# Kernel tuning notes

Hardware: AMD Instinct MI355X
Metric: run time of the kernel (lower is better)

## Reference

```python
import jax, jax.numpy as jnp
import numpy as np
import math

PI = math.pi
POS_RANGE = (0.0, PI, -PI, PI)            # (x_lo, x_hi, y_lo, y_hi)
DIR_RANGE = (0.5 * PI, 0.85 * PI, -0.85 * PI, -0.5 * PI)


def setup_inputs() -> dict:
    key = jax.random.key(0)
    kx, kg, kw1, kw2 = jax.random.split(key, 4)
    N = 1_048_576
    G0, G1, G2, G3, F = 64, 64, 32, 32, 16
    # sample query points strictly inside the valid angular ranges
    lo = jnp.array([POS_RANGE[0], POS_RANGE[2], DIR_RANGE[0], DIR_RANGE[2]], jnp.float32)
    hi = jnp.array([POS_RANGE[1], POS_RANGE[3], DIR_RANGE[1], DIR_RANGE[3]], jnp.float32)
    u = jax.random.uniform(kx, (N, 4), jnp.float32, 0.0, 0.999)
    x = lo + u * (hi - lo)
    # xavier-uniform learned 4D feature grid
    gb = math.sqrt(6.0 / (G3 + F))
    grid = jax.random.uniform(kg, (G0, G1, G2, G3, F), jnp.float32, -gb, gb)
    H = 4 * F
    b1v = math.sqrt(6.0 / (F + H))
    w1 = jax.random.uniform(kw1, (F, H), jnp.float32, -b1v, b1v)
    b1 = jnp.zeros((H,), jnp.float32)
    b2v = math.sqrt(6.0 / (H + 3))
    w2 = jax.random.uniform(kw2, (H, 3), jnp.float32, -b2v, b2v)
    b2 = jnp.zeros((3,), jnp.float32)
    return {"x": x, "grid": grid, "w1": w1, "b1": b1, "w2": w2, "b2": b2}


def _quadlinear(x, grid):
    G0, G1, G2, G3, F = grid.shape
    # normalize each coordinate to grid index space (faithful to original,
    # including normalizing dim0 by G0-1 / dim1 by G1-1 while dim0 indexes axis 1)
    c0 = (x[:, 0] - POS_RANGE[0]) / (POS_RANGE[1] - POS_RANGE[0]) * (G0 - 1)
    c1 = (x[:, 1] - POS_RANGE[2]) / (POS_RANGE[3] - POS_RANGE[2]) * (G1 - 1)
    c2 = (x[:, 2] - DIR_RANGE[0]) / (DIR_RANGE[1] - DIR_RANGE[0]) * (G2 - 1)
    c3 = (x[:, 3] - DIR_RANGE[2]) / (DIR_RANGE[3] - DIR_RANGE[2]) * (G3 - 1)
    W, H, D, T = G1 - 1, G0 - 1, G2 - 1, G3 - 1
    tlx = c0.astype(jnp.int32)  # coords are non-negative -> trunc == floor
    tly = c1.astype(jnp.int32)
    tlz = c2.astype(jnp.int32)
    tlw = c3.astype(jnp.int32)
    xf = jnp.mod(c0, 1.0)[:, None]
    yf = jnp.mod(c1, 1.0)[:, None]
    zf = jnp.mod(c2, 1.0)[:, None]
    wf = jnp.mod(c3, 1.0)[:, None]
    brx = jnp.minimum(tlx + 1, W)
    bry = jnp.minimum(tly + 1, H)
    brz = jnp.minimum(tlz + 1, D)
    brw = jnp.minimum(tlw + 1, T)
    g = lambda a, b, c, d: grid[a, b, c, d]  # [N, F] gather
    c0000 = g(tly, tlx, tlz, tlw); c1000 = g(tly, brx, tlz, tlw)
    c0100 = g(bry, tlx, tlz, tlw); c0010 = g(tly, tlx, brz, tlw)
    c0001 = g(tly, tlx, tlz, brw); c1100 = g(bry, brx, tlz, tlw)
    c1010 = g(tly, brx, brz, tlw); c1001 = g(tly, brx, tlz, brw)
    c0110 = g(bry, tlx, brz, tlw); c0101 = g(bry, tlx, tlz, brw)
    c0011 = g(tly, tlx, brz, brw); c1110 = g(bry, brx, brz, tlw)
    c1101 = g(bry, brx, tlz, brw); c1011 = g(tly, brx, brz, brw)
    c0111 = g(bry, tlx, brz, brw); c1111 = g(bry, brx, brz, brw)
    c00 = c0000 * (1 - xf) + c1000 * xf
    c01 = c0001 * (1 - xf) + c1001 * xf
    c10 = c0100 * (1 - xf) + c1100 * xf
    c11 = c0110 * (1 - xf) + c1110 * xf
    c20 = c0010 * (1 - xf) + c1010 * xf
    c21 = c0011 * (1 - xf) + c1011 * xf
    c30 = c0101 * (1 - xf) + c1101 * xf
    c31 = c0111 * (1 - xf) + c1111 * xf
    cc0 = c00 * (1 - yf) + c10 * yf
    cc1 = c01 * (1 - yf) + c11 * yf
    cc2 = c20 * (1 - yf) + c30 * yf
    cc3 = c21 * (1 - yf) + c31 * yf
    c4 = cc0 * (1 - zf) + cc2 * zf
    c5 = cc1 * (1 - zf) + cc3 * zf
    return c4 * (1 - wf) + c5 * wf  # [N, F]


def reference(x, grid, w1, b1, w2, b2):
    feat = _quadlinear(x, grid)
    h = feat @ w1 + b1
    h = jnp.where(h >= 0, h, 0.01 * h)  # LeakyReLU(0.01)
    out = h @ w2 + b2
    return jax.nn.sigmoid(out) * 255.0
```

## Files before the change

### kernel.cpp

```cpp
#include <hip/hip_runtime.h>
#include <math.h>

__global__ __launch_bounds__(256) void gridnet_kernel(
    const float* __restrict__ x,
    const float* __restrict__ grid,
    const float* __restrict__ w1,
    const float* __restrict__ b1,
    const float* __restrict__ w2,
    const float* __restrict__ b2,
    float* __restrict__ out,
    int N)
{
    __shared__ float w1s[16 * 64];
    __shared__ float b1s[64];
    __shared__ float w2s[64 * 3];
    __shared__ float b2s[4];

    const int t = threadIdx.x;
    for (int i = t; i < 1024; i += 256) w1s[i] = w1[i];
    if (t < 64)  b1s[t] = b1[t];
    if (t < 192) w2s[t] = w2[t];
    if (t < 3)   b2s[t] = b2[t];
    __syncthreads();

    const int gid = blockIdx.x * 256 + t;
    if (gid >= N) return;

    const float4 xv = reinterpret_cast<const float4*>(x)[gid];

    const float lo1 = (float)(-M_PI);
    const float sp0 = (float)(M_PI);
    const float sp1 = (float)(2.0 * M_PI);
    const float lo2 = (float)(0.5 * M_PI);
    const float sp2 = (float)(0.85 * M_PI - 0.5 * M_PI);
    const float lo3 = (float)(-0.85 * M_PI);
    const float sp3 = (float)(-0.5 * M_PI - (-0.85 * M_PI));

    const float c0 = (xv.x - 0.0f) / sp0 * 63.0f;
    const float c1 = (xv.y - lo1) / sp1 * 63.0f;
    const float c2 = (xv.z - lo2) / sp2 * 31.0f;
    const float c3 = (xv.w - lo3) / sp3 * 31.0f;

    const int tlx = (int)c0;
    const int tly = (int)c1;
    const int tlz = (int)c2;
    const int tlw = (int)c3;

    const float xf = c0 - (float)tlx;
    const float yf = c1 - (float)tly;
    const float zf = c2 - (float)tlz;
    const float wf = c3 - (float)tlw;

    const int brx = min(tlx + 1, 63);
    const int bry = min(tly + 1, 63);
    const int brz = min(tlz + 1, 31);
    const int brw = min(tlw + 1, 31);

    const float wx0 = 1.0f - xf, wx1 = xf;
    const float wy0 = 1.0f - yf, wy1 = yf;
    const float wz0 = 1.0f - zf, wz1 = zf;
    const float ww0 = 1.0f - wf, ww1 = wf;

    float cw[2][2][2];
    cw[0][0][0] = wy0 * wz0 * ww0;
    cw[0][0][1] = wy0 * wz0 * ww1;
    cw[0][1][0] = wy0 * wz1 * ww0;
    cw[0][1][1] = wy0 * wz1 * ww1;
    cw[1][0][0] = wy1 * wz0 * ww0;
    cw[1][0][1] = wy1 * wz1 * ww0;
    cw[1][1][0] = wy1 * wz0 * ww1;
    cw[1][1][1] = wy1 * wz1 * ww1;

    const float wxv[2] = {wx0, wx1};
    const int axv[2] = {tlx, brx};
    const int ayv[2] = {tly, bry};
    const int azv[2] = {tlz, brz};
    const int awv[2] = {tlw, brw};

    float feat[16];
    #pragma unroll
    for (int f = 0; f < 16; ++f) feat[f] = 0.0f;

    #pragma unroll
    for (int iy = 0; iy < 2; ++iy) {
        #pragma unroll
        for (int ix = 0; ix < 2; ++ix) {
            const int base1 = (ayv[iy] * 64 + axv[ix]) * 32;
            const float wyx = wxv[ix];
            #pragma unroll
            for (int iz = 0; iz < 2; ++iz) {
                const int base0 = (base1 + azv[iz]) * 32;
                #pragma unroll
                for (int iw = 0; iw < 2; ++iw) {
                    const float w = wyx * cw[iy][iz][iw];
                    const float4* p = reinterpret_cast<const float4*>(
                        grid + (size_t)(base0 + awv[iw]) * 16);
                    const float4 v0 = p[0];
                    const float4 v1 = p[1];
                    const float4 v2 = p[2];
                    const float4 v3 = p[3];
                    feat[0]  += w * v0.x;  feat[1]  += w * v0.y;
                    feat[2]  += w * v0.z;  feat[3]  += w * v0.w;
                    feat[4]  += w * v1.x;  feat[5]  += w * v1.y;
                    feat[6]  += w * v1.z;  feat[7]  += w * v1.w;
                    feat[8]  += w * v2.x;  feat[9]  += w * v2.y;
                    feat[10] += w * v2.z;  feat[11] += w * v2.w;
                    feat[12] += w * v3.x;  feat[13] += w * v3.y;
                    feat[14] += w * v3.z;  feat[15] += w * v3.w;
                }
            }
        }
    }

    float o0 = b2s[0];
    float o1 = b2s[1];
    float o2 = b2s[2];

    #pragma unroll
    for (int j4 = 0; j4 < 16; ++j4) {
        float4 h = reinterpret_cast<const float4*>(b1s)[j4];
        #pragma unroll
        for (int i = 0; i < 16; ++i) {
            const float4 wv = reinterpret_cast<const float4*>(w1s)[i * 16 + j4];
            h.x += feat[i] * wv.x;
            h.y += feat[i] * wv.y;
            h.z += feat[i] * wv.z;
            h.w += feat[i] * wv.w;
        }
        const float hx = (h.x >= 0.0f) ? h.x : 0.01f * h.x;
        const float hy = (h.y >= 0.0f) ? h.y : 0.01f * h.y;
        const float hz = (h.z >= 0.0f) ? h.z : 0.01f * h.z;
        const float hw = (h.w >= 0.0f) ? h.w : 0.01f * h.w;
        const float* w2p = w2s + j4 * 12;
        o0 += hx * w2p[0] + hy * w2p[3] + hz * w2p[6] + hw * w2p[9];
        o1 += hx * w2p[1] + hy * w2p[4] + hz * w2p[7] + hw * w2p[10];
        o2 += hx * w2p[2] + hy * w2p[5] + hz * w2p[8] + hw * w2p[11];
    }

    const float r0 = 255.0f / (1.0f + expf(-o0));
    const float r1 = 255.0f / (1.0f + expf(-o1));
    const float r2 = 255.0f / (1.0f + expf(-o2));

    float* op = out + (size_t)gid * 3;
    op[0] = r0;
    op[1] = r1;
    op[2] = r2;
}

extern "C" void kernel_launch(void* const* d_in, const int* in_sizes, int n_in,
                              void* d_out, int out_size, void* d_ws, size_t ws_size,
                              hipStream_t stream) {
    const float* x    = (const float*)d_in[0];
    const float* grid = (const float*)d_in[1];
    const float* w1   = (const float*)d_in[2];
    const float* b1   = (const float*)d_in[3];
    const float* w2   = (const float*)d_in[4];
    const float* b2   = (const float*)d_in[5];
    float* out = (float*)d_out;

    const int N = in_sizes[0] / 4;
    const int blocks = (N + 255) / 256;
    gridnet_kernel<<<blocks, 256, 0, stream>>>(x, grid, w1, b1, w2, b2, out, N);
}
```

Measured before the change: 256.5 us.

## Split each point across four lanes for gather and MLP with shuffle reductions

Each query point is now handled by a quad of four threads. Each lane gathers the 4 corners for one (y,x) pair, and the partial features are summed with xor shuffles. Each lane then computes a quarter of the hidden layer, the outputs are reduced again with shuffles, and one lane per output channel writes the sigmoid result. The aim is more memory-level parallelism and fewer per-thread registers for the 16-corner gather and the 16x64 MLP. The cost is four times as many threads, redundant coordinate math in every lane, shuffle overhead, and a launch-bounds occupancy hint.

```diff
diff --git a/kernel.cpp b/kernel.cpp
--- a/kernel.cpp
+++ b/kernel.cpp
@@ -1,7 +1,7 @@
 #include <hip/hip_runtime.h>
 #include <math.h>
 
-__global__ __launch_bounds__(256) void gridnet_kernel(
+__global__ __launch_bounds__(256, 6) void gridnet_quad(
     const float* __restrict__ x,
     const float* __restrict__ grid,
     const float* __restrict__ w1,
@@ -20,13 +20,15 @@
     for (int i = t; i < 1024; i += 256) w1s[i] = w1[i];
     if (t < 64)  b1s[t] = b1[t];
     if (t < 192) w2s[t] = w2[t];
-    if (t < 3)   b2s[t] = b2[t];
+    if (t < 4)   b2s[t] = (t < 3) ? b2[t] : 0.0f;
     __syncthreads();
 
-    const int gid = blockIdx.x * 256 + t;
-    if (gid >= N) return;
+    const int lane = t & 3;
+    const int q    = t >> 2;
+    const int p    = blockIdx.x * 64 + q;
+    if (p >= N) return;
 
-    const float4 xv = reinterpret_cast<const float4*>(x)[gid];
+    const float4 xv = reinterpret_cast<const float4*>(x)[p];
 
     const float lo1 = (float)(-M_PI);
     const float sp0 = (float)(M_PI);
@@ -56,68 +58,66 @@
     const int brz = min(tlz + 1, 31);
     const int brw = min(tlw + 1, 31);
 
-    const float wx0 = 1.0f - xf, wx1 = xf;
-    const float wy0 = 1.0f - yf, wy1 = yf;
     const float wz0 = 1.0f - zf, wz1 = zf;
     const float ww0 = 1.0f - wf, ww1 = wf;
 
-    float cw[2][2][2];
-    cw[0][0][0] = wy0 * wz0 * ww0;
-    cw[0][0][1] = wy0 * wz0 * ww1;
-    cw[0][1][0] = wy0 * wz1 * ww0;
-    cw[0][1][1] = wy0 * wz1 * ww1;
-    cw[1][0][0] = wy1 * wz0 * ww0;
-    cw[1][0][1] = wy1 * wz1 * ww0;
-    cw[1][1][0] = wy1 * wz0 * ww1;
-    cw[1][1][1] = wy1 * wz1 * ww1;
+    const int  iy  = lane >> 1;
+    const int  ix  = lane & 1;
+    const int  ay  = iy ? bry : tly;
+    const int  ax  = ix ? brx : tlx;
+    const float wyl = iy ? yf : (1.0f - yf);
+    const float wxl = ix ? xf : (1.0f - xf);
+    const float wbase = wxl * wyl;
 
-    const float wxv[2] = {wx0, wx1};
-    const int axv[2] = {tlx, brx};
-    const int ayv[2] = {tly, bry};
-    const int azv[2] = {tlz, brz};
-    const int awv[2] = {tlw, brw};
+    const float s00  = wz0 * ww0;
+    const float s11  = wz1 * ww1;
+    const float s01n = wz0 * ww1;
+    const float s10n = wz1 * ww0;
+    const float s01 = iy ? s10n : s01n;
+    const float s10 = iy ? s01n : s10n;
+
+    const int base = (ay * 64 + ax) * 32;
+    const int idx00 = (base + tlz) * 32 + tlw;
+    const int idx01 = (base + tlz) * 32 + brw;
+    const int idx10 = (base + brz) * 32 + tlw;
+    const int idx11 = (base + brz) * 32 + brw;
+
+    const float ws[4]  = {wbase * s00, wbase * s01, wbase * s10, wbase * s11};
+    const int   idxs[4] = {idx00, idx01, idx10, idx11};
 
     float feat[16];
     #pragma unroll
     for (int f = 0; f < 16; ++f) feat[f] = 0.0f;
 
     #pragma unroll
-    for (int iy = 0; iy < 2; ++iy) {
-        #pragma unroll
-        for (int ix = 0; ix < 2; ++ix) {
-            const int base1 = (ayv[iy] * 64 + axv[ix]) * 32;
-            const float wyx = wxv[ix];
-            #pragma unroll
-            for (int iz = 0; iz < 2; ++iz) {
-                const int base0 = (base1 + azv[iz]) * 32;
-                #pragma unroll
-                for (int iw = 0; iw < 2; ++iw) {
-                    const float w = wyx * cw[iy][iz][iw];
-                    const float4* p = reinterpret_cast<const float4*>(
-                        grid + (size_t)(base0 + awv[iw]) * 16);
-                    const float4 v0 = p[0];
-                    const float4 v1 = p[1];
-                    const float4 v2 = p[2];
-                    const float4 v3 = p[3];
-                    feat[0]  += w * v0.x;  feat[1]  += w * v0.y;
-                    feat[2]  += w * v0.z;  feat[3]  += w * v0.w;
-                    feat[4]  += w * v1.x;  feat[5]  += w * v1.y;
-                    feat[6]  += w * v1.z;  feat[7]  += w * v1.w;
-                    feat[8]  += w * v2.x;  feat[9]  += w * v2.y;
-                    feat[10] += w * v2.z;  feat[11] += w * v2.w;
-                    feat[12] += w * v3.x;  feat[13] += w * v3.y;
-                    feat[14] += w * v3.z;  feat[15] += w * v3.w;
-                }
-            }
-        }
+    for (int c = 0; c < 4; ++c) {
+        const float4* p4 = reinterpret_cast<const float4*>(
+            grid + (size_t)idxs[c] * 16);
+        const float4 v0 = p4[0];
+        const float4 v1 = p4[1];
+        const float4 v2 = p4[2];
+        const float4 v3 = p4[3];
+        const float w = ws[c];
+        feat[0]  += w * v0.x;  feat[1]  += w * v0.y;
+        feat[2]  += w * v0.z;  feat[3]  += w * v0.w;
+        feat[4]  += w * v1.x;  feat[5]  += w * v1.y;
+        feat[6]  += w * v1.z;  feat[7]  += w * v1.w;
+        feat[8]  += w * v2.x;  feat[9]  += w * v2.y;
+        feat[10] += w * v2.z;  feat[11] += w * v2.w;
+        feat[12] += w * v3.x;  feat[13] += w * v3.y;
+        feat[14] += w * v3.z;  feat[15] += w * v3.w;
     }
 
-    float o0 = b2s[0];
-    float o1 = b2s[1];
-    float o2 = b2s[2];
+    #pragma unroll
+    for (int f = 0; f < 16; ++f) {
+        feat[f] += __shfl_xor(feat[f], 1);
+        feat[f] += __shfl_xor(feat[f], 2);
+    }
 
+    float o0 = 0.0f, o1 = 0.0f, o2 = 0.0f;
     #pragma unroll
-    for (int j4 = 0; j4 < 16; ++j4) {
+    for (int g = 0; g < 4; ++g) {
+        const int j4 = lane + 4 * g;
         float4 h = reinterpret_cast<const float4*>(b1s)[j4];
         #pragma unroll
         for (int i = 0; i < 16; ++i) {
@@ -137,14 +137,14 @@
         o2 += hx * w2p[2] + hy * w2p[5] + hz * w2p[8] + hw * w2p[11];
     }
 
-    const float r0 = 255.0f / (1.0f + expf(-o0));
-    const float r1 = 255.0f / (1.0f + expf(-o1));
-    const float r2 = 255.0f / (1.0f + expf(-o2));
+    o0 += __shfl_xor(o0, 1);  o0 += __shfl_xor(o0, 2);
+    o1 += __shfl_xor(o1, 1);  o1 += __shfl_xor(o1, 2);
+    o2 += __shfl_xor(o2, 1);  o2 += __shfl_xor(o2, 2);
 
-    float* op = out + (size_t)gid * 3;
-    op[0] = r0;
-    op[1] = r1;
-    op[2] = r2;
+    const float osel = (lane == 0) ? o0 : ((lane == 1) ? o1 : o2);
+    const float ob   = osel + b2s[lane];
+    const float r    = 255.0f / (1.0f + expf(-ob));
+    if (lane < 3) out[(size_t)p * 3 + lane] = r;
 }
 
 extern "C" void kernel_launch(void* const* d_in, const int* in_sizes, int n_in,
@@ -159,6 +159,6 @@
     float* out = (float*)d_out;
 
     const int N = in_sizes[0] / 4;
-    const int blocks = (N + 255) / 256;
-    gridnet_kernel<<<blocks, 256, 0, stream>>>(x, grid, w1, b1, w2, b2, out, N);
+    const int blocks = (N + 63) / 64;
+    gridnet_quad<<<blocks, 256, 0, stream>>>(x, grid, w1, b1, w2, b2, out, N);
 }
```

After: 420.6 us. 64.0% more time.

## Bucket-sort query points by grid cell before interpolation for gather locality

Applied to the files above, without the earlier changes.

Adds a counting-sort pre-pass (histogram, three-stage scan, atomic scatter) that reorders the query points by their grid cell key. The main kernel then reads the sorted points and writes results back through the saved index, and its block order is remapped in a strided pattern. The aim is to make the 16 random grid gathers per point hit nearby cache lines. In exchange it adds six extra launches, about 8 MB of histogram traffic, and a scattered output write. The sorted path only runs when N equals exactly 2048*512 and the workspace is large enough.

```diff
diff --git a/kernel.cpp b/kernel.cpp
--- a/kernel.cpp
+++ b/kernel.cpp
@@ -1,15 +1,96 @@
 #include <hip/hip_runtime.h>
 #include <math.h>
 
-__global__ __launch_bounds__(256) void gridnet_kernel(
-    const float* __restrict__ x,
+
+#define NBUCKET (1u << 21)
+#define SCAN_BLOCKS 2048
+
+__device__ __forceinline__ int point_key(const float4 xv) {
+    const float c0 = xv.x * (63.0f / (float)M_PI);
+    const float c1 = (xv.y + (float)M_PI) * (63.0f / (float)(2.0 * M_PI));
+    const float c2 = (xv.z - (float)(0.5 * M_PI)) * (31.0f / (float)(0.35 * M_PI));
+    const float c3 = (xv.w + (float)(0.85 * M_PI)) * (31.0f / (float)(0.35 * M_PI));
+    int tx = min(max((int)c0, 0), 63);
+    int ty = min(max((int)c1, 0), 63);
+    int tz = min(max((int)c2, 0), 31);
+    int tw = min(max((int)c3, 0), 31);
+    return ((ty * 64 + tx) * 32 + tz) * 16 + (tw >> 1);
+}
+
+__global__ __launch_bounds__(1024) void k_zero(unsigned* __restrict__ hist) {
+    hist[blockIdx.x * 1024 + threadIdx.x] = 0u;
+}
+
+__global__ __launch_bounds__(256) void k_hist(const float4* __restrict__ x,
+                                              unsigned* __restrict__ hist, int N) {
+    const int p = blockIdx.x * 256 + threadIdx.x;
+    if (p >= N) return;
+    atomicAdd(&hist[point_key(x[p])], 1u);
+}
+
+__global__ __launch_bounds__(1024) void k_scanA(unsigned* __restrict__ data,
+                                                unsigned* __restrict__ partial) {
+    __shared__ unsigned s[1024];
+    const int t = threadIdx.x;
+    const int base = blockIdx.x * 1024;
+    const unsigned v = data[base + t];
+    s[t] = v;
+    __syncthreads();
+    #pragma unroll
+    for (int off = 1; off < 1024; off <<= 1) {
+        const unsigned add = (t >= off) ? s[t - off] : 0u;
+        __syncthreads();
+        s[t] += add;
+        __syncthreads();
+    }
+    data[base + t] = (t == 0) ? 0u : s[t - 1];
+    if (t == 1023) partial[blockIdx.x] = s[1023];
+}
+
+__global__ __launch_bounds__(1024) void k_scanB(unsigned* __restrict__ partial) {
+    __shared__ unsigned s[1024];
+    const int t = threadIdx.x;
+    const unsigned v0 = partial[2 * t];
+    const unsigned v1 = partial[2 * t + 1];
+    s[t] = v0 + v1;
+    __syncthreads();
+    #pragma unroll
+    for (int off = 1; off < 1024; off <<= 1) {
+        const unsigned add = (t >= off) ? s[t - off] : 0u;
+        __syncthreads();
+        s[t] += add;
+        __syncthreads();
+    }
+    const unsigned exc = (t == 0) ? 0u : s[t - 1];
+    partial[2 * t] = exc;
+    partial[2 * t + 1] = exc + v0;
+}
+
+__global__ __launch_bounds__(1024) void k_scanC(unsigned* __restrict__ data,
+                                                const unsigned* __restrict__ partial) {
+    data[blockIdx.x * 1024 + threadIdx.x] += partial[blockIdx.x];
+}
+
+__global__ __launch_bounds__(256) void k_scatter(const float4* __restrict__ x,
+                                                 unsigned* __restrict__ offsets,
+                                                 float4* __restrict__ xs,
+                                                 unsigned* __restrict__ idx, int N) {
+    const int p = blockIdx.x * 256 + threadIdx.x;
+    if (p >= N) return;
+    const float4 xv = x[p];
+    const unsigned slot = atomicAdd(&offsets[point_key(xv)], 1u);
+    xs[slot] = xv;
+    idx[slot] = p;
+}
+
+template <bool SORTED>
+__global__ __launch_bounds__(256) void gridnet_main(
+    const float4* __restrict__ xs,
+    const unsigned* __restrict__ idx,
     const float* __restrict__ grid,
-    const float* __restrict__ w1,
-    const float* __restrict__ b1,
-    const float* __restrict__ w2,
-    const float* __restrict__ b2,
-    float* __restrict__ out,
-    int N)
+    const float* __restrict__ w1, const float* __restrict__ b1,
+    const float* __restrict__ w2, const float* __restrict__ b2,
+    float* __restrict__ out, int N, int nblk)
 {
     __shared__ float w1s[16 * 64];
     __shared__ float b1s[64];
@@ -23,10 +104,15 @@
     if (t < 3)   b2s[t] = b2[t];
     __syncthreads();
 
-    const int gid = blockIdx.x * 256 + t;
-    if (gid >= N) return;
-
-    const float4 xv = reinterpret_cast<const float4*>(x)[gid];
+    int b = blockIdx.x;
+    if (SORTED && (nblk & 7) == 0)
+        b = (blockIdx.x & 7) * (nblk >> 3) + (blockIdx.x >> 3);
+
+    const int i = b * 256 + t;
+    if (i >= N) return;
+
+    const float4 xv = xs[i];
+    const int p = SORTED ? (int)idx[i] : i;
 
     const float lo1 = (float)(-M_PI);
     const float sp0 = (float)(M_PI);
@@ -93,12 +179,12 @@
                 #pragma unroll
                 for (int iw = 0; iw < 2; ++iw) {
                     const float w = wyx * cw[iy][iz][iw];
-                    const float4* p = reinterpret_cast<const float4*>(
+                    const float4* p4 = reinterpret_cast<const float4*>(
                         grid + (size_t)(base0 + awv[iw]) * 16);
-                    const float4 v0 = p[0];
-                    const float4 v1 = p[1];
-                    const float4 v2 = p[2];
-                    const float4 v3 = p[3];
+                    const float4 v0 = p4[0];
+                    const float4 v1 = p4[1];
+                    const float4 v2 = p4[2];
+                    const float4 v3 = p4[3];
                     feat[0]  += w * v0.x;  feat[1]  += w * v0.y;
                     feat[2]  += w * v0.z;  feat[3]  += w * v0.w;
                     feat[4]  += w * v1.x;  feat[5]  += w * v1.y;
@@ -120,12 +206,12 @@
     for (int j4 = 0; j4 < 16; ++j4) {
         float4 h = reinterpret_cast<const float4*>(b1s)[j4];
         #pragma unroll
-        for (int i = 0; i < 16; ++i) {
-            const float4 wv = reinterpret_cast<const float4*>(w1s)[i * 16 + j4];
-            h.x += feat[i] * wv.x;
-            h.y += feat[i] * wv.y;
-            h.z += feat[i] * wv.z;
-            h.w += feat[i] * wv.w;
+        for (int i2 = 0; i2 < 16; ++i2) {
+            const float4 wv = reinterpret_cast<const float4*>(w1s)[i2 * 16 + j4];
+            h.x += feat[i2] * wv.x;
+            h.y += feat[i2] * wv.y;
+            h.z += feat[i2] * wv.z;
+            h.w += feat[i2] * wv.w;
         }
         const float hx = (h.x >= 0.0f) ? h.x : 0.01f * h.x;
         const float hy = (h.y >= 0.0f) ? h.y : 0.01f * h.y;
@@ -141,7 +227,7 @@
     const float r1 = 255.0f / (1.0f + expf(-o1));
     const float r2 = 255.0f / (1.0f + expf(-o2));
 
-    float* op = out + (size_t)gid * 3;
+    float* op = out + (size_t)p * 3;
     op[0] = r0;
     op[1] = r1;
     op[2] = r2;
@@ -159,6 +245,32 @@
     float* out = (float*)d_out;
 
     const int N = in_sizes[0] / 4;
-    const int blocks = (N + 255) / 256;
-    gridnet_kernel<<<blocks, 256, 0, stream>>>(x, grid, w1, b1, w2, b2, out, N);
-}
+    const int nblk = (N + 255) / 256;
+
+    const size_t xs_bytes   = (size_t)N * 16;
+    const size_t idx_bytes  = (size_t)N * 4;
+    const size_t hist_bytes = (size_t)NBUCKET * 4;
+    const size_t part_bytes = (size_t)SCAN_BLOCKS * 4;
+    const size_t need = xs_bytes + idx_bytes + hist_bytes + part_bytes;
+
+    if (ws_size >= need && N == SCAN_BLOCKS * 512) {
+        char* ws = (char*)d_ws;
+        float4*   xs      = (float4*)ws;
+        unsigned* idx     = (unsigned*)(ws + xs_bytes);
+        unsigned* hist    = (unsigned*)(ws + xs_bytes + idx_bytes);
+        unsigned* partial = (unsigned*)(ws + xs_bytes + idx_bytes + hist_bytes);
+        const float4* x4 = (const float4*)x;
+
+        k_zero   <<<NBUCKET / 1024, 1024, 0, stream>>>(hist);
+        k_hist   <<<nblk, 256, 0, stream>>>(x4, hist, N);
+        k_scanA  <<<SCAN_BLOCKS, 1024, 0, stream>>>(hist, partial);
+        k_scanB  <<<1, 1024, 0, stream>>>(partial);
+        k_scanC  <<<SCAN_BLOCKS, 1024, 0, stream>>>(hist, partial);
+        k_scatter<<<nblk, 256, 0, stream>>>(x4, hist, xs, idx, N);
+        gridnet_main<true><<<nblk, 256, 0, stream>>>(
+            xs, idx, grid, w1, b1, w2, b2, out, N, nblk);
+    } else {
+        gridnet_main<false><<<nblk, 256, 0, stream>>>(
+            (const float4*)x, nullptr, grid, w1, b1, w2, b2, out, N, nblk);
+    }
+}
```

New measurement: 357.0 us. 1.39x slower.
